# Optimization experiments

Measured on AMD Instinct MI355X. Metric: run time of the kernel, lower is better.

## Reference

```python
import jax, jax.numpy as jnp
import numpy as np

GRID = (192, 96, 192)
NUM_MATERIALS = 8
WORLD_SCALE = 2.0
OCC_THRESHOLD = 0.01
TEMPERATURE = 1.0


def _look_at(eye, target, up):
    eye = np.asarray(eye, np.float32); target = np.asarray(target, np.float32); up = np.asarray(up, np.float32)
    f = target - eye; f = f / np.linalg.norm(f)
    r = np.cross(f, up); r = r / np.linalg.norm(r)
    u = np.cross(r, f)
    view = np.eye(4, dtype=np.float32)
    view[0, :3] = r;  view[0, 3] = -r @ eye
    view[1, :3] = u;  view[1, 3] = -u @ eye
    view[2, :3] = -f; view[2, 3] = f @ eye
    return view


def _perspective(fov_deg, aspect, near, far):
    f = 1.0 / np.tan(np.radians(fov_deg) / 2.0)
    p = np.zeros((4, 4), dtype=np.float32)
    p[0, 0] = f / aspect
    p[1, 1] = f
    p[2, 2] = (far + near) / (near - far)
    p[2, 3] = 2.0 * far * near / (near - far)
    p[3, 2] = -1.0
    return p


def setup_inputs() -> dict:
    key = jax.random.key(0)
    k1, k2 = jax.random.split(key)
    X, Y, Z = GRID
    occupancy_logits = jax.random.normal(k1, (X, Y, Z), dtype=jnp.float32)
    material_logits = jax.random.normal(k2, (X, Y, Z, NUM_MATERIALS), dtype=jnp.float32)
    # grid world extent: x,z in [-X/2, X/2]*scale, y in [0, Y]*scale
    camera_view = jnp.asarray(_look_at(eye=(0.0, 250.0, 700.0), target=(0.0, 96.0, 0.0), up=(0.0, 1.0, 0.0)))
    camera_proj = jnp.asarray(_perspective(60.0, 1.0, 0.1, 2000.0))
    return {
        'occupancy_logits': occupancy_logits,
        'material_logits': material_logits,
        'camera_view': camera_view,
        'camera_proj': camera_proj,
        'max_blocks': 100000,
    }


def _voxel_centers(X, Y, Z):
    # centers = (idx + 0.5 + offset) * world_scale, offset = (-X/2, 0, -Z/2)
    cx = (jnp.arange(X, dtype=jnp.float32) + 0.5 - X / 2.0) * WORLD_SCALE
    cy = (jnp.arange(Y, dtype=jnp.float32) + 0.5) * WORLD_SCALE
    cz = (jnp.arange(Z, dtype=jnp.float32) + 0.5 - Z / 2.0) * WORLD_SCALE
    gx, gy, gz = jnp.meshgrid(cx, cy, cz, indexing='ij')
    return jnp.stack([gx.ravel(), gy.ravel(), gz.ravel()], axis=-1)  # (N, 3)


def reference(occupancy_logits, material_logits, camera_view, camera_proj, max_blocks):
    X, Y, Z = occupancy_logits.shape
    N = X * Y * Z
    occ = jax.nn.sigmoid(occupancy_logits).reshape(-1)          # (N,)
    active = occ > OCC_THRESHOLD                                # torch.nonzero -> mask

    centers = _voxel_centers(X, Y, Z)                           # (N, 3) world centers

    # frustum test in NDC (world_to_clip with combined MVP)
    mvp = camera_proj @ camera_view                             # (4, 4)
    clip = centers @ mvp[:, :3].T + mvp[:, 3]                   # (N, 4)
    w = jnp.maximum(clip[:, 3], 1e-6)
    ndc = clip[:, :3] / w[:, None]
    visible = jnp.all((ndc >= -1.0) & (ndc <= 1.0), axis=-1)

    valid = active & visible

    # depth-based top-k: keep max_blocks nearest valid voxels
    view_z = centers @ camera_view[2, :3] + camera_view[2, 3]
    depth = jnp.maximum(-view_z, 0.0)
    score = jnp.where(valid, -depth, -jnp.inf)                  # nearest first
    _, idx = jax.lax.top_k(score, max_blocks)
    keep = jnp.zeros((N,), dtype=bool).at[idx].set(valid[idx])  # pruned_mask scatter

    pruned_weights = jnp.where(keep, occ, 0.0).reshape(X, Y, Z)

    # render prep: per-voxel material distribution scaled by occupancy weight
    mat_probs = jax.nn.softmax(material_logits / TEMPERATURE, axis=-1)
    return pruned_weights[..., None] * mat_probs                # (X, Y, Z, M)
```

## Files before the change

### kernel.cpp

```cpp
#include <hip/hip_runtime.h>

#define GX 192
#define GY 96
#define GZ 192
#define GRP (GY*GZ)
#define NVOX (GX*GRP)

#define NXC 12
#define XCW (GX/NXC)
#define GBLK (GRP/256)
#define CSTR 16

#define K2T 1024
#define GPT (GRP/K2T)
#define WBINS 4096
#define BPT (WBINS/K2T)

#define WS_MVP    0
#define WS_DEPTH  64
#define WS_CNT8   (WS_DEPTH + GRP*4)
#define WS_SEL    (WS_CNT8 + GRP*CSTR)
#define WS_TLIST  (WS_SEL + 16)
#define WS_TPREF  (WS_TLIST + 1024)
#define WS_NTIED  (WS_TPREF + GX*4)

typedef float f4 __attribute__((ext_vector_type(4)));

__device__ __forceinline__ bool voxel_valid(int x, int g,
                                            const float* __restrict__ occL,
                                            const float* M,
                                            float* occ_out)
{
    int y = g / GZ;
    int z = g - y * GZ;
    float cx = (float)(2 * x - 191);
    float cy = (float)(2 * y + 1);
    float cz = (float)(2 * z - 191);

    float logit = occL[(size_t)x * GRP + g];
    float occ = 1.0f / (1.0f + expf(-logit));
    *occ_out = occ;
    if (!(occ > 0.01f)) return false;

    float c0 = __fadd_rn(__fmaf_rn(cz, M[2],  __fmaf_rn(cy, M[1],  __fmul_rn(cx, M[0]))),  M[3]);
    float c1 = __fadd_rn(__fmaf_rn(cz, M[6],  __fmaf_rn(cy, M[5],  __fmul_rn(cx, M[4]))),  M[7]);
    float c2 = __fadd_rn(__fmaf_rn(cz, M[10], __fmaf_rn(cy, M[9],  __fmul_rn(cx, M[8]))),  M[11]);
    float c3 = __fadd_rn(__fmaf_rn(cz, M[14], __fmaf_rn(cy, M[13], __fmul_rn(cx, M[12]))), M[15]);

    float w  = fmaxf(c3, 1e-6f);
    float nx = c0 / w;
    float ny = c1 / w;
    float nz = c2 / w;
    return (nx >= -1.0f) && (nx <= 1.0f) &&
           (ny >= -1.0f) && (ny <= 1.0f) &&
           (nz >= -1.0f) && (nz <= 1.0f);
}

__device__ __forceinline__ void compute_mvp_lds(const float* view, const float* proj,
                                                float* s_mvp, int tid)
{
    if (tid < 16) {
        int r = tid >> 2, c = tid & 3;
        float acc = 0.0f;
        for (int k = 0; k < 4; ++k)
            acc = __fadd_rn(acc, __fmul_rn(proj[r * 4 + k], view[k * 4 + c]));
        s_mvp[tid] = acc;
    }
}

__device__ __forceinline__ unsigned wave_incl_scan(unsigned v, int lane)
{
    #pragma unroll
    for (int off = 1; off < 64; off <<= 1) {
        unsigned u = (unsigned)__shfl_up((int)v, off);
        if (lane >= off) v += u;
    }
    return v;
}

__global__ __launch_bounds__(256) void k_prep_count(
    const float* __restrict__ view, const float* __restrict__ proj,
    const float* __restrict__ occL,
    float* __restrict__ mvpOut,
    unsigned* __restrict__ depthBits,
    unsigned char* __restrict__ cnt8)
{
    __shared__ float s_mvp[16];
    int tid = threadIdx.x;
    compute_mvp_lds(view, proj, s_mvp, tid);
    __syncthreads();

    int b  = blockIdx.x;
    int gb = b % GBLK;
    int xc = b / GBLK;
    int g  = gb * 256 + tid;

    if (b == 0 && tid < 16) mvpOut[tid] = s_mvp[tid];

    if (xc == 0) {
        int y = g / GZ;
        int z = g - y * GZ;
        float cy = (float)(2 * y + 1);
        float cz = (float)(2 * z - 191);
        float seed = __fmul_rn(-191.0f, view[8]);
        float vz = __fadd_rn(__fmaf_rn(cz, view[10], __fmaf_rn(cy, view[9], seed)), view[11]);
        float d  = fmaxf(-vz, 0.0f);
        depthBits[g] = __float_as_uint(d);
    }

    unsigned c = 0;
    int x0 = xc * XCW;
    for (int x = x0; x < x0 + XCW; ++x) {
        float occ;
        if (voxel_valid(x, g, occL, s_mvp, &occ)) ++c;
    }
    cnt8[(size_t)g * CSTR + xc] = (unsigned char)c;
}

__global__ __launch_bounds__(1024) void k_select(
    const float* __restrict__ view, const float* __restrict__ proj,
    const float* __restrict__ occL,
    const unsigned* __restrict__ depthBits,
    const unsigned char* __restrict__ cnt8,
    const int* __restrict__ maxBlocksPtr,
    unsigned* __restrict__ sel,
    unsigned* __restrict__ tiedList,
    unsigned* __restrict__ tiedPrefX,
    unsigned* __restrict__ nTiedG)
{
    __shared__ float s_mvp[16];
    __shared__ unsigned s_h[WBINS];
    __shared__ unsigned s_w[16];
    __shared__ unsigned s_wT[16], s_wMn[16], s_wMx[16];
    __shared__ unsigned s_tot, s_mn, s_mx, s_chTot;
    __shared__ unsigned s_found, s_prefix, s_remK;
    __shared__ unsigned s_list[256];
    __shared__ int s_n;
    __shared__ unsigned s_cntX[GX];

    int tid  = threadIdx.x;
    int lane = tid & 63;
    int wid  = tid >> 6;
    compute_mvp_lds(view, proj, s_mvp, tid);

    unsigned d[GPT], c[GPT];
    #pragma unroll
    for (int k = 0; k < GPT; ++k) {
        int g = tid + k * K2T;
        d[k] = depthBits[g];
        const unsigned* cp = (const unsigned*)(cnt8 + (size_t)g * CSTR);
        unsigned w0 = cp[0], w1 = cp[1], w2 = cp[2];
        unsigned s = (w0 & 255u) + ((w0 >> 8) & 255u) + ((w0 >> 16) & 255u) + (w0 >> 24);
        s += (w1 & 255u) + ((w1 >> 8) & 255u) + ((w1 >> 16) & 255u) + (w1 >> 24);
        s += (w2 & 255u) + ((w2 >> 8) & 255u) + ((w2 >> 16) & 255u) + (w2 >> 24);
        c[k] = s;
    }

    unsigned tot = 0, mn = 0xFFFFFFFFu, mx = 0;
    #pragma unroll
    for (int k = 0; k < GPT; ++k) {
        tot += c[k];
        if (c[k]) {
            unsigned hi = d[k] >> 16;
            mn = min(mn, hi);
            mx = max(mx, hi);
        }
    }
    for (int m = 1; m < 64; m <<= 1) {
        tot += (unsigned)__shfl_xor((int)tot, m);
        mn = min(mn, (unsigned)__shfl_xor((int)mn, m));
        mx = max(mx, (unsigned)__shfl_xor((int)mx, m));
    }
    if (lane == 0) { s_wT[wid] = tot; s_wMn[wid] = mn; s_wMx[wid] = mx; }
    __syncthreads();
    if (tid == 0) {
        unsigned t2 = 0, m2 = 0xFFFFFFFFu, x2 = 0;
        for (int w = 0; w < 16; ++w) {
            t2 += s_wT[w]; m2 = min(m2, s_wMn[w]); x2 = max(x2, s_wMx[w]);
        }
        s_tot = t2; s_mn = m2; s_mx = x2;
        s_found = 0;
    }
    __syncthreads();
    unsigned K = (unsigned)maxBlocksPtr[0];
    tot = s_tot; mn = s_mn; mx = s_mx;

    if (tot <= K) {
        if (tid == 0) {
            sel[0] = 0xFFFFFFFFu;
            sel[1] = 0x7FFFFFFFu;
            *nTiedG = 0u;
        }
        return;
    }

    unsigned remK = K;
    unsigned prefix = 0;
    unsigned span = mx - mn + 1u;
    unsigned nchunks = (span + WBINS - 1u) / WBINS;
    for (unsigned ch = 0; ch < nchunks; ++ch) {
        unsigned base = mn + ch * WBINS;
        #pragma unroll
        for (int j = 0; j < BPT; ++j) s_h[tid + j * K2T] = 0;
        __syncthreads();
        #pragma unroll
        for (int k = 0; k < GPT; ++k) {
            if (c[k]) {
                unsigned hi = d[k] >> 16;
                if (hi >= base && hi < base + WBINS)
                    atomicAdd(&s_h[hi - base], c[k]);
            }
        }
        __syncthreads();
        unsigned ps = 0;
        #pragma unroll
        for (int j = 0; j < BPT; ++j) ps += s_h[tid * BPT + j];
        unsigned iw = wave_incl_scan(ps, lane);
        if (lane == 63) s_w[wid] = iw;
        __syncthreads();
        if (wid == 0) {
            unsigned wv = (lane < 16) ? s_w[lane] : 0u;
            unsigned wiw = wave_incl_scan(wv, lane);
            if (lane < 16) s_w[lane] = wiw - wv;
            if (lane == 15) s_chTot = wiw;
        }
        __syncthreads();
        unsigned incl = iw + s_w[wid];
        unsigned chunkTot = s_chTot;
        unsigned excl = incl - ps;
        if (remK <= chunkTot && excl < remK && remK <= incl) {
            unsigned cum = excl;
            #pragma unroll
            for (int j = 0; j < BPT; ++j) {
                unsigned hv = s_h[tid * BPT + j];
                if (cum < remK && remK <= cum + hv) {
                    s_found  = 1u;
                    s_prefix = base + (unsigned)(tid * BPT + j);
                    s_remK   = remK - cum;
                }
                cum += hv;
            }
        }
        __syncthreads();
        if (s_found) { prefix = s_prefix; remK = s_remK; break; }
        remK -= chunkTot;
        __syncthreads();
    }

    for (int p = 0; p < 2; ++p) {
        int matchShift = (p == 0) ? 16 : 8;
        int digitShift = (p == 0) ? 8 : 0;
        if (tid < 256) s_h[tid] = 0;
        __syncthreads();
        #pragma unroll
        for (int k = 0; k < GPT; ++k) {
            if (c[k] && (d[k] >> matchShift) == prefix)
                atomicAdd(&s_h[(d[k] >> digitShift) & 255u], c[k]);
        }
        __syncthreads();
        unsigned ps = (tid < 256) ? s_h[tid] : 0u;
        unsigned iw = wave_incl_scan(ps, lane);
        if (lane == 63) s_w[wid] = iw;
        __syncthreads();
        if (wid == 0) {
            unsigned wv = (lane < 16) ? s_w[lane] : 0u;
            unsigned wiw = wave_incl_scan(wv, lane);
            if (lane < 16) s_w[lane] = wiw - wv;
        }
        __syncthreads();
        unsigned incl = iw + s_w[wid];
        unsigned excl = incl - ps;
        if (excl < remK && remK <= incl) {
            s_prefix = (prefix << 8) | (unsigned)tid;
            s_remK   = remK - excl;
        }
        __syncthreads();
        prefix = s_prefix; remK = s_remK;
        __syncthreads();
    }
    unsigned T = prefix;
    unsigned R = remK;

    if (tid == 0) s_n = 0;
    for (int x = tid; x < GX; x += K2T) s_cntX[x] = 0;
    __syncthreads();
    #pragma unroll
    for (int k = 0; k < GPT; ++k) {
        if (d[k] == T) {
            int idx = atomicAdd(&s_n, 1);
            if (idx < 256) s_list[idx] = (unsigned)(tid + k * K2T);
        }
    }
    __syncthreads();
    int n = min(s_n, 256);
    if (tid == 0) {
        for (int a = 1; a < n; ++a) {
            unsigned v = s_list[a];
            int b = a - 1;
            while (b >= 0 && s_list[b] > v) { s_list[b + 1] = s_list[b]; --b; }
            s_list[b + 1] = v;
        }
    }
    __syncthreads();
    int pairs = GX * n;
    for (int pr = tid; pr < pairs; pr += K2T) {
        int x = pr / n;
        int s = pr - x * n;
        float occ;
        if (voxel_valid(x, (int)s_list[s], occL, s_mvp, &occ))
            atomicAdd(&s_cntX[x], 1u);
    }
    __syncthreads();
    if (tid == 0) {
        unsigned run = 0;
        for (int x = 0; x < GX; ++x) { tiedPrefX[x] = run; run += s_cntX[x]; }
        *nTiedG = (unsigned)n;
        sel[0] = T;
        sel[1] = R;
    }
    if (tid < n) tiedList[tid] = s_list[tid];
}

__global__ __launch_bounds__(256) void k_out(
    const float* __restrict__ occL,
    const float* __restrict__ matL,
    const float* __restrict__ mvp,
    const unsigned* __restrict__ depthBits,
    const unsigned* __restrict__ sel,
    const unsigned* __restrict__ tiedList,
    const unsigned* __restrict__ tiedPrefX,
    const unsigned* __restrict__ nTiedPtr,
    float* __restrict__ out)
{
    int i = blockIdx.x * 256 + threadIdx.x;
    if (i >= NVOX) return;
    int x = i / GRP;
    int g = i - x * GRP;

    float occ;
    bool valid = voxel_valid(x, g, occL, mvp, &occ);
    bool keep = false;
    if (valid) {
        unsigned T  = sel[0];
        unsigned db = depthBits[g];
        if (db < T) {
            keep = true;
        } else if (db == T) {
            unsigned R = sel[1];
            unsigned rank = tiedPrefX[x];
            int n = (int)*nTiedPtr;
            for (int s = 0; s < n; ++s) {
                unsigned gs = tiedList[s];
                if (gs >= (unsigned)g) break;
                float o2;
                if (voxel_valid(x, (int)gs, occL, mvp, &o2)) ++rank;
            }
            keep = rank < R;
        }
    }

    f4 o0 = (f4)(0.0f);
    f4 o1 = (f4)(0.0f);
    if (keep) {
        const f4* mp = reinterpret_cast<const f4*>(matL) + (size_t)i * 2;
        f4 a = __builtin_nontemporal_load(mp);
        f4 b = __builtin_nontemporal_load(mp + 1);
        float mx = fmaxf(fmaxf(fmaxf(a[0], a[1]), fmaxf(a[2], a[3])),
                         fmaxf(fmaxf(b[0], b[1]), fmaxf(b[2], b[3])));
        float e0 = expf(a[0] - mx), e1 = expf(a[1] - mx), e2 = expf(a[2] - mx), e3 = expf(a[3] - mx);
        float e4 = expf(b[0] - mx), e5 = expf(b[1] - mx), e6 = expf(b[2] - mx), e7 = expf(b[3] - mx);
        float s = ((e0 + e1) + (e2 + e3)) + ((e4 + e5) + (e6 + e7));
        float inv = occ / s;
        o0[0] = e0 * inv; o0[1] = e1 * inv; o0[2] = e2 * inv; o0[3] = e3 * inv;
        o1[0] = e4 * inv; o1[1] = e5 * inv; o1[2] = e6 * inv; o1[3] = e7 * inv;
    }
    f4* op = reinterpret_cast<f4*>(out) + (size_t)i * 2;
    __builtin_nontemporal_store(o0, op);
    __builtin_nontemporal_store(o1, op + 1);
}

extern "C" void kernel_launch(void* const* d_in, const int* in_sizes, int n_in,
                              void* d_out, int out_size, void* d_ws, size_t ws_size,
                              hipStream_t stream)
{
    const float* occL = (const float*)d_in[0];
    const float* matL = (const float*)d_in[1];
    const float* view = (const float*)d_in[2];
    const float* proj = (const float*)d_in[3];
    const int*   mb   = (const int*)d_in[4];

    char* ws = (char*)d_ws;
    float*         mvp      = (float*)(ws + WS_MVP);
    unsigned*      depthB   = (unsigned*)(ws + WS_DEPTH);
    unsigned char* cnt8     = (unsigned char*)(ws + WS_CNT8);
    unsigned*      sel      = (unsigned*)(ws + WS_SEL);
    unsigned*      tiedList = (unsigned*)(ws + WS_TLIST);
    unsigned*      tiedPref = (unsigned*)(ws + WS_TPREF);
    unsigned*      nTied    = (unsigned*)(ws + WS_NTIED);

    k_prep_count<<<NXC * GBLK, 256, 0, stream>>>(view, proj, occL, mvp, depthB, cnt8);
    k_select<<<1, K2T, 0, stream>>>(view, proj, occL, depthB, cnt8, mb,
                                    sel, tiedList, tiedPref, nTied);
    k_out<<<NVOX / 256, 256, 0, stream>>>(occL, matL, mvp, depthB, sel,
                                          tiedList, tiedPref, nTied, (float*)d_out);
}
```

Measured before the change: 64.11 us.

## Store per-voxel validity bitmask in prep pass and reuse it downstream

The prep kernel now writes a 16-bit validity mask per column chunk instead of a per-chunk count. The select and output kernels read bits from this mask instead of recomputing the sigmoid and frustum test for every voxel, including inside the tie-ranking loop. The output kernel only reads the occupancy logit and computes the sigmoid for kept voxels, and its material loads are no longer nontemporal. This trades recomputation and full occupancy reads in the output pass for a small mask buffer (about 0.9 MB) that is read with a stride.

```diff
diff --git a/kernel.cpp b/kernel.cpp
--- a/kernel.cpp
+++ b/kernel.cpp
@@ -9,7 +9,6 @@
 #define NXC 12
 #define XCW (GX/NXC)
 #define GBLK (GRP/256)
-#define CSTR 16
 
 #define K2T 1024
 #define GPT (GRP/K2T)
@@ -18,8 +17,8 @@
 
 #define WS_MVP    0
 #define WS_DEPTH  64
-#define WS_CNT8   (WS_DEPTH + GRP*4)
-#define WS_SEL    (WS_CNT8 + GRP*CSTR)
+#define WS_MASK   (WS_DEPTH + GRP*4)
+#define WS_SEL    (WS_MASK + NXC*GRP*2)
 #define WS_TLIST  (WS_SEL + 16)
 #define WS_TPREF  (WS_TLIST + 1024)
 #define WS_NTIED  (WS_TPREF + GX*4)
@@ -83,7 +82,7 @@
     const float* __restrict__ occL,
     float* __restrict__ mvpOut,
     unsigned* __restrict__ depthBits,
-    unsigned char* __restrict__ cnt8)
+    unsigned short* __restrict__ mask16)
 {
     __shared__ float s_mvp[16];
     int tid = threadIdx.x;
@@ -108,27 +107,25 @@
         depthBits[g] = __float_as_uint(d);
     }
 
-    unsigned c = 0;
+    unsigned m = 0;
     int x0 = xc * XCW;
-    for (int x = x0; x < x0 + XCW; ++x) {
+    #pragma unroll
+    for (int j = 0; j < XCW; ++j) {
         float occ;
-        if (voxel_valid(x, g, occL, s_mvp, &occ)) ++c;
-    }
-    cnt8[(size_t)g * CSTR + xc] = (unsigned char)c;
+        if (voxel_valid(x0 + j, g, occL, s_mvp, &occ)) m |= (1u << j);
+    }
+    mask16[(size_t)xc * GRP + g] = (unsigned short)m;
 }
 
 __global__ __launch_bounds__(1024) void k_select(
-    const float* __restrict__ view, const float* __restrict__ proj,
-    const float* __restrict__ occL,
     const unsigned* __restrict__ depthBits,
-    const unsigned char* __restrict__ cnt8,
+    const unsigned short* __restrict__ mask16,
     const int* __restrict__ maxBlocksPtr,
     unsigned* __restrict__ sel,
     unsigned* __restrict__ tiedList,
     unsigned* __restrict__ tiedPrefX,
     unsigned* __restrict__ nTiedG)
 {
-    __shared__ float s_mvp[16];
     __shared__ unsigned s_h[WBINS];
     __shared__ unsigned s_w[16];
     __shared__ unsigned s_wT[16], s_wMn[16], s_wMx[16];
@@ -141,19 +138,17 @@
     int tid  = threadIdx.x;
     int lane = tid & 63;
     int wid  = tid >> 6;
-    compute_mvp_lds(view, proj, s_mvp, tid);
 
     unsigned d[GPT], c[GPT];
     #pragma unroll
     for (int k = 0; k < GPT; ++k) {
         int g = tid + k * K2T;
         d[k] = depthBits[g];
-        const unsigned* cp = (const unsigned*)(cnt8 + (size_t)g * CSTR);
-        unsigned w0 = cp[0], w1 = cp[1], w2 = cp[2];
-        unsigned s = (w0 & 255u) + ((w0 >> 8) & 255u) + ((w0 >> 16) & 255u) + (w0 >> 24);
-        s += (w1 & 255u) + ((w1 >> 8) & 255u) + ((w1 >> 16) & 255u) + (w1 >> 24);
-        s += (w2 & 255u) + ((w2 >> 8) & 255u) + ((w2 >> 16) & 255u) + (w2 >> 24);
-        c[k] = s;
+        unsigned cc = 0;
+        #pragma unroll
+        for (int xc = 0; xc < NXC; ++xc)
+            cc += __popc((unsigned)mask16[(size_t)xc * GRP + g]);
+        c[k] = cc;
     }
 
     unsigned tot = 0, mn = 0xFFFFFFFFu, mx = 0;
@@ -306,8 +301,8 @@
     for (int pr = tid; pr < pairs; pr += K2T) {
         int x = pr / n;
         int s = pr - x * n;
-        float occ;
-        if (voxel_valid(x, (int)s_list[s], occL, s_mvp, &occ))
+        unsigned gs = s_list[s];
+        if ((mask16[(size_t)(x >> 4) * GRP + gs] >> (x & 15)) & 1u)
             atomicAdd(&s_cntX[x], 1u);
     }
     __syncthreads();
@@ -324,8 +319,8 @@
 __global__ __launch_bounds__(256) void k_out(
     const float* __restrict__ occL,
     const float* __restrict__ matL,
-    const float* __restrict__ mvp,
     const unsigned* __restrict__ depthBits,
+    const unsigned short* __restrict__ mask16,
     const unsigned* __restrict__ sel,
     const unsigned* __restrict__ tiedList,
     const unsigned* __restrict__ tiedPrefX,
@@ -337,8 +332,7 @@
     int x = i / GRP;
     int g = i - x * GRP;
 
-    float occ;
-    bool valid = voxel_valid(x, g, occL, mvp, &occ);
+    bool valid = (mask16[(size_t)(x >> 4) * GRP + g] >> (x & 15)) & 1u;
     bool keep = false;
     if (valid) {
         unsigned T  = sel[0];
@@ -352,8 +346,7 @@
             for (int s = 0; s < n; ++s) {
                 unsigned gs = tiedList[s];
                 if (gs >= (unsigned)g) break;
-                float o2;
-                if (voxel_valid(x, (int)gs, occL, mvp, &o2)) ++rank;
+                rank += (mask16[(size_t)(x >> 4) * GRP + gs] >> (x & 15)) & 1u;
             }
             keep = rank < R;
         }
@@ -362,9 +355,11 @@
     f4 o0 = (f4)(0.0f);
     f4 o1 = (f4)(0.0f);
     if (keep) {
+        float logit = occL[i];
+        float occ = 1.0f / (1.0f + expf(-logit));
         const f4* mp = reinterpret_cast<const f4*>(matL) + (size_t)i * 2;
-        f4 a = __builtin_nontemporal_load(mp);
-        f4 b = __builtin_nontemporal_load(mp + 1);
+        f4 a = mp[0];
+        f4 b = mp[1];
         float mx = fmaxf(fmaxf(fmaxf(a[0], a[1]), fmaxf(a[2], a[3])),
                          fmaxf(fmaxf(b[0], b[1]), fmaxf(b[2], b[3])));
         float e0 = expf(a[0] - mx), e1 = expf(a[1] - mx), e2 = expf(a[2] - mx), e3 = expf(a[3] - mx);
@@ -390,17 +385,16 @@
     const int*   mb   = (const int*)d_in[4];
 
     char* ws = (char*)d_ws;
-    float*         mvp      = (float*)(ws + WS_MVP);
-    unsigned*      depthB   = (unsigned*)(ws + WS_DEPTH);
-    unsigned char* cnt8     = (unsigned char*)(ws + WS_CNT8);
-    unsigned*      sel      = (unsigned*)(ws + WS_SEL);
-    unsigned*      tiedList = (unsigned*)(ws + WS_TLIST);
-    unsigned*      tiedPref = (unsigned*)(ws + WS_TPREF);
-    unsigned*      nTied    = (unsigned*)(ws + WS_NTIED);
-
-    k_prep_count<<<NXC * GBLK, 256, 0, stream>>>(view, proj, occL, mvp, depthB, cnt8);
-    k_select<<<1, K2T, 0, stream>>>(view, proj, occL, depthB, cnt8, mb,
-                                    sel, tiedList, tiedPref, nTied);
-    k_out<<<NVOX / 256, 256, 0, stream>>>(occL, matL, mvp, depthB, sel,
+    float*          mvp      = (float*)(ws + WS_MVP);
+    unsigned*       depthB   = (unsigned*)(ws + WS_DEPTH);
+    unsigned short* mask16   = (unsigned short*)(ws + WS_MASK);
+    unsigned*       sel      = (unsigned*)(ws + WS_SEL);
+    unsigned*       tiedList = (unsigned*)(ws + WS_TLIST);
+    unsigned*       tiedPref = (unsigned*)(ws + WS_TPREF);
+    unsigned*       nTied    = (unsigned*)(ws + WS_NTIED);
+
+    k_prep_count<<<NXC * GBLK, 256, 0, stream>>>(view, proj, occL, mvp, depthB, mask16);
+    k_select<<<1, K2T, 0, stream>>>(depthB, mask16, mb, sel, tiedList, tiedPref, nTied);
+    k_out<<<NVOX / 256, 256, 0, stream>>>(occL, matL, depthB, mask16, sel,
                                           tiedList, tiedPref, nTied, (float*)d_out);
 }
```

Result: slower. 81.85 us (+27.7%).
